# Performance work log

Hardware: AMD Instinct MI355X
Metric: run time of the kernel (lower is better)

## Reference

```python
import jax, jax.numpy as jnp
import numpy as np

N_NODES = 156
NFEAT = 256
NHID = 128
B = 16384
T = 24
HLSTM = 32
ALPHA = 0.2


def setup_inputs() -> dict:
    key = jax.random.key(0)
    ks = jax.random.split(key, 16)
    f32 = jnp.float32
    inp = {
        "embedding": jax.random.normal(ks[0], (N_NODES, NFEAT), f32),
        "x": jax.random.normal(ks[1], (B, T, N_NODES), f32),
        "adj": jax.random.randint(ks[2], (N_NODES, N_NODES), 0, 2, jnp.int32),
        # GAT params (xavier-ish scale)
        "W_recent": jax.random.normal(ks[3], (NFEAT, NHID), f32) * 0.08,
        "a_recent": jax.random.normal(ks[4], (2 * NHID, 1), f32) * 0.1,
        "W_period": jax.random.normal(ks[5], (NFEAT, NHID), f32) * 0.08,
        "a_period": jax.random.normal(ks[6], (2 * NHID, 1), f32) * 0.1,
        # LSTM params, torch layout: weight_ih [4H, D], weight_hh [4H, H]
        "Wih_r": jax.random.normal(ks[7], (4 * HLSTM, N_NODES), f32) * 0.08,
        "Whh_r": jax.random.normal(ks[8], (4 * HLSTM, HLSTM), f32) * 0.08,
        "bih_r": jnp.zeros((4 * HLSTM,), f32),
        "bhh_r": jnp.zeros((4 * HLSTM,), f32),
        "Wih_p": jax.random.normal(ks[9], (4 * HLSTM, N_NODES), f32) * 0.08,
        "Whh_p": jax.random.normal(ks[10], (4 * HLSTM, HLSTM), f32) * 0.08,
        "bih_p": jnp.zeros((4 * HLSTM,), f32),
        "bhh_p": jnp.zeros((4 * HLSTM,), f32),
        "fc_W": jax.random.normal(ks[11], (N_NODES, 2 * HLSTM), f32) * 0.1,
        "fc_b": jnp.zeros((N_NODES,), f32),
    }
    return inp


def _gat_attention(embedding, W, a, adj):
    # h = embedding @ W : [N, F]
    h = embedding @ W
    F = h.shape[1]
    # e[i,j] = leakyrelu(h_i . a[:F] + h_j . a[F:])  (same math as the
    # repeat/cat construction, without materializing [N*N, 2F])
    s1 = h @ a[:F, 0]   # [N]
    s2 = h @ a[F:, 0]   # [N]
    e = jax.nn.leaky_relu(s1[:, None] + s2[None, :], ALPHA)
    e = jnp.where(adj > 0, e, jnp.float32(-9e15))
    return jax.nn.softmax(e, axis=1)  # [N, N]


def _lstm_last(x_seq, Wih, Whh, bih, bhh):
    # x_seq: [B, T, D]; returns last hidden state [B, H]
    H = Whh.shape[1]
    Bn = x_seq.shape[0]
    h0 = jnp.zeros((Bn, H), x_seq.dtype)
    c0 = jnp.zeros((Bn, H), x_seq.dtype)
    bias = bih + bhh

    def step(carry, xt):
        h, c = carry
        g = xt @ Wih.T + h @ Whh.T + bias
        i, f, gg, o = jnp.split(g, 4, axis=-1)  # torch gate order i,f,g,o
        c = jax.nn.sigmoid(f) * c + jax.nn.sigmoid(i) * jnp.tanh(gg)
        h = jax.nn.sigmoid(o) * jnp.tanh(c)
        return (h, c), None

    (h, c), _ = jax.lax.scan(step, (h0, c0), jnp.swapaxes(x_seq, 0, 1))
    return h


def reference(embedding, x, adj, W_recent, a_recent, W_period, a_period,
              Wih_r, Whh_r, bih_r, bhh_r, Wih_p, Whh_p, bih_p, bhh_p,
              fc_W, fc_b):
    recent = x[:, :4, :]   # [B, 4, N]
    period = x[:, 4:, :]   # [B, T-4, N]

    # attention depends only on embedding/adj -> identical across timesteps
    attn_r = _gat_attention(embedding, W_recent, a_recent, adj)  # [N, N]
    attn_p = _gat_attention(embedding, W_period, a_period, adj)

    # out[b,t,i] = sum_j attn[i,j] * x[b,t,j]
    xr = jnp.einsum('ij,btj->bti', attn_r, recent)
    xp = jnp.einsum('ij,btj->bti', attn_p, period)

    hr = _lstm_last(xr, Wih_r, Whh_r, bih_r, bhh_r)  # [B, 32]
    hp = _lstm_last(xp, Wih_p, Whh_p, bih_p, bhh_p)  # [B, 32]

    h = jnp.concatenate([hr, hp], axis=1)            # [B, 64]
    return h @ fc_W.T + fc_b                         # [B, 156]
```

## Files before the change

### kernel.cpp

```cpp
#include <hip/hip_runtime.h>
#include <hip/hip_bf16.h>
#include <math.h>

#define N_NODES 156
#define NFEAT 256
#define NHID 128
#define BATCH 16384
#define TT 24
#define HLSTM 32
#define G4 128
#define ALPHA 0.2f
#define XSTRIDE (TT*N_NODES)
#define SLOTF 2496

typedef __attribute__((ext_vector_type(8))) short bf16x8;
typedef __attribute__((ext_vector_type(4))) float f32x4;

static __device__ __forceinline__ unsigned short f2bf(float f) {
    unsigned u = __float_as_uint(f);
    u += 0x7fffu + ((u >> 16) & 1u);
    return (unsigned short)(u >> 16);
}
static __device__ __forceinline__ bf16x8 cv8(float4 a, float4 b) {
    union { __hip_bfloat16 h[8]; bf16x8 v; } u;
    u.h[0] = __float2bfloat16(a.x); u.h[1] = __float2bfloat16(a.y);
    u.h[2] = __float2bfloat16(a.z); u.h[3] = __float2bfloat16(a.w);
    u.h[4] = __float2bfloat16(b.x); u.h[5] = __float2bfloat16(b.y);
    u.h[6] = __float2bfloat16(b.z); u.h[7] = __float2bfloat16(b.w);
    return u.v;
}
static __device__ __forceinline__ float sigm(float x) { return 1.f / (1.f + __expf(-x)); }
static __device__ __forceinline__ float tanh_(float x) { return 1.f - 2.f / (__expf(2.f * x) + 1.f); }

__global__ void k_gat_s(const float* __restrict__ emb,
                        const float* __restrict__ Wr, const float* __restrict__ ar,
                        const float* __restrict__ Wp, const float* __restrict__ ap,
                        float* __restrict__ s_buf ) {
    int i = blockIdx.x;
    int gat = blockIdx.y;
    const float* W = gat ? Wp : Wr;
    const float* a = gat ? ap : ar;
    int j = threadIdx.x;
    __shared__ float erow[NFEAT];
    __shared__ float red[128];
    for (int k = j; k < NFEAT; k += 128) erow[k] = emb[i*NFEAT + k];
    __syncthreads();
    float h = 0.f;
    for (int k = 0; k < NFEAT; ++k) h = fmaf(erow[k], W[k*NHID + j], h);
    float v1 = h * a[j];
    float v2 = h * a[NHID + j];
    red[j] = v1; __syncthreads();
    for (int s = 64; s > 0; s >>= 1) { if (j < s) red[j] += red[j+s]; __syncthreads(); }
    if (j == 0) s_buf[(gat*2+0)*N_NODES + i] = red[0];
    __syncthreads();
    red[j] = v2; __syncthreads();
    for (int s = 64; s > 0; s >>= 1) { if (j < s) red[j] += red[j+s]; __syncthreads(); }
    if (j == 0) s_buf[(gat*2+1)*N_NODES + i] = red[0];
}

__global__ void k_attn(const float* __restrict__ s_buf, const int* __restrict__ adj,
                       float* __restrict__ attn ) {
    int i = blockIdx.x, gat = blockIdx.y;
    int j = threadIdx.x;
    __shared__ float red[256];
    float s1 = s_buf[(gat*2+0)*N_NODES + i];
    bool act = (j < N_NODES);
    float e = -INFINITY;
    if (act) {
        float s2 = s_buf[(gat*2+1)*N_NODES + j];
        float z = s1 + s2;
        z = (z > 0.f) ? z : ALPHA * z;
        if (adj[i*N_NODES + j] <= 0) z = -9e15f;
        e = z;
    }
    red[j] = e; __syncthreads();
    for (int s = 128; s > 0; s >>= 1) { if (j < s) red[j] = fmaxf(red[j], red[j+s]); __syncthreads(); }
    float m = red[0]; __syncthreads();
    float val = act ? __expf(e - m) : 0.f;
    red[j] = val; __syncthreads();
    for (int s = 128; s > 0; s >>= 1) { if (j < s) red[j] += red[j+s]; __syncthreads(); }
    float inv = 1.f / red[0];
    if (act) attn[(gat*N_NODES + i)*N_NODES + j] = val * inv;
}

__global__ void k_prep(const float* __restrict__ attn,
                       const float* __restrict__ Wih_r, const float* __restrict__ Wih_p,
                       const float* __restrict__ Whh_r, const float* __restrict__ Whh_p,
                       const float* __restrict__ bih_r, const float* __restrict__ bhh_r,
                       const float* __restrict__ bih_p, const float* __restrict__ bhh_p,
                       unsigned short* __restrict__ Mbf ,
                       unsigned short* __restrict__ Whhbf ,
                       float* __restrict__ bias2 ) {
    int g = blockIdx.x, gat = blockIdx.y;
    const float* Wih = gat ? Wih_p : Wih_r;
    const float* A = attn + gat*N_NODES*N_NODES;
    int j = threadIdx.x;
    if (j < 160) {
        float acc = 0.f;
        if (j < N_NODES)
            for (int n = 0; n < N_NODES; ++n)
                acc = fmaf(Wih[g*N_NODES + n], A[n*N_NODES + j], acc);
        Mbf[(gat*G4 + g)*160 + j] = f2bf(acc);
    }
    if (j < HLSTM)
        Whhbf[(gat*G4 + g)*HLSTM + j] = f2bf((gat ? Whh_p : Whh_r)[g*HLSTM + j]);
    if (g == 0 && j < G4)
        bias2[gat*G4 + j] = gat ? (bih_p[j] + bhh_p[j]) : (bih_r[j] + bhh_r[j]);
}

__global__ void __launch_bounds__(128, 2)
k_fused(const float* __restrict__ x,
        const unsigned short* __restrict__ Mbf,
        const unsigned short* __restrict__ Whhbf,
        const float* __restrict__ bias2,
        const float* __restrict__ fcW,
        const float* __restrict__ fcb,
        float* __restrict__ out) {
    __shared__ __align__(16) float xsf[3][SLOTF];
    __shared__ __align__(16) unsigned short hfrag[512];
    __shared__ __align__(16) float P_ls[512];
    __shared__ __align__(16) unsigned short hcat[16*72];

    const int tid = threadIdx.x;
    const int w  = tid >> 6;
    const int l  = tid & 63;
    const int lm = l & 15;
    const int lg = l >> 4;
    const int b0 = blockIdx.x * 16;
    const float* xg = x + (size_t)b0 * XSTRIDE;

    unsigned goff[5];
    #pragma unroll
    for (int k = 0; k < 5; ++k) {
        int c = l + (w*5 + k)*64;
        if (c > 623) c = 623;
        int r = c / 39;
        goff[k] = (unsigned)(r*XSTRIDE + (c - r*39)*4);
    }

    bf16x8 bfr[4][5];
    bf16x8 wrec[4];
    float  bias_v[4];
    float  cst[8];
    unsigned short hrv[8], hpv[8];
    const int nbase = w ? 2 : 0;
    const float4 f4z = make_float4(0.f, 0.f, 0.f, 0.f);

#define LOAD_FRAGS(Mb, Wb, bs) do {                                          \
    _Pragma("unroll")                                                        \
    for (int nt = 0; nt < 4; ++nt) {                                         \
        int ntid = nbase + (nt & 1) + ((nt >> 1) << 2);                      \
        int n_ = ntid*16 + lm;                                               \
        _Pragma("unroll")                                                    \
        for (int kf = 0; kf < 5; ++kf)                                       \
            bfr[nt][kf] = *(const bf16x8*)((Mb) + n_*160 + kf*32 + lg*8);    \
        wrec[nt]   = *(const bf16x8*)((Wb) + n_*HLSTM + lg*8);               \
        bias_v[nt] = (bs)[n_];                                               \
    } } while (0)

#define DMA_STEP(S_, T_) do {                                                 \
    const float* gp_ = xg + (size_t)(T_)*N_NODES;                             \
    _Pragma("unroll")                                                         \
    for (int k_ = 0; k_ < 5; ++k_) {                                          \
        if (w*5 + k_ != 9 || l < 48)                                          \
            __builtin_amdgcn_global_load_lds(                                 \
                (const __attribute__((address_space(1))) void*)(gp_ + goff[k_]), \
                (__attribute__((address_space(3))) void*)(&xsf[S_][(w*5 + k_)*256]), \
                16, 0, 0);                                                    \
    } } while (0)

#define WAITVM(N_) asm volatile("s_waitcnt vmcnt(" #N_ ")" ::: "memory")
#define LGKM0()    asm volatile("s_waitcnt lgkmcnt(0)" ::: "memory")

    DMA_STEP(0, 0);
    LOAD_FRAGS(Mbf, Whhbf, bias2);
    DMA_STEP(1, 1);
    DMA_STEP(2, 2);

    if (w == 1) {
        #pragma unroll
        for (int ds = 0; ds < 2; ++ds)
            #pragma unroll
            for (int i = 0; i < 4; ++i) {
                hfrag[((lm>>3) + 2*ds)*128 + (lg*4 + i)*8 + (lm&7)] = 0;
                cst[ds*4 + i] = 0.f;
            }
    }

#define STEP(T_, S_, ISS_) do {                                               \
    LGKM0();                                                                  \
    __builtin_amdgcn_s_barrier();   \
    const float* xr_ = &xsf[S_][0] + lm*N_NODES + lg*8;                       \
    float4 q0_[5], q1_[5];                                                    \
    _Pragma("unroll")                                                         \
    for (int kf = 0; kf < 5; ++kf) {                                          \
        q0_[kf] = *(const float4*)(xr_ + kf*32);                              \
        q1_[kf] = *(const float4*)(xr_ + kf*32 + 4);                          \
    }                                                                         \
    bf16x8 hf_ = *(const bf16x8*)(hfrag + l*8);                               \
    if (lg == 3) q1_[4] = f4z;                       \
    bf16x8 af_[5];                                                            \
    _Pragma("unroll")                                                         \
    for (int kf = 0; kf < 5; ++kf) af_[kf] = cv8(q0_[kf], q1_[kf]);           \
    f32x4 acc[4];                                                             \
    _Pragma("unroll")                                                         \
    for (int nt = 0; nt < 4; ++nt)                                            \
        acc[nt] = (f32x4){bias_v[nt], bias_v[nt], bias_v[nt], bias_v[nt]};    \
    _Pragma("unroll")                                                         \
    for (int kf = 0; kf < 5; ++kf)                                            \
        _Pragma("unroll")                                                     \
        for (int nt = 0; nt < 4; ++nt)                                        \
            acc[nt] = __builtin_amdgcn_mfma_f32_16x16x32_bf16(af_[kf], bfr[nt][kf], acc[nt], 0, 0, 0); \
    _Pragma("unroll")                                                         \
    for (int nt = 0; nt < 4; ++nt)                                            \
        acc[nt] = __builtin_amdgcn_mfma_f32_16x16x32_bf16(hf_, wrec[nt], acc[nt], 0, 0, 0); \
    float sa_[8], sb_[8];                                                     \
    if (w == 0) {                                                             \
        _Pragma("unroll")                                                     \
        for (int ds = 0; ds < 2; ++ds)                                        \
            _Pragma("unroll")                                                 \
            for (int i = 0; i < 4; ++i) {                                     \
                float si = sigm(acc[ds][i]);                                  \
                float tg = tanh_(acc[2 + ds][i]);                             \
                P_ls[(ds*4 + i)*64 + l] = si * tg;                            \
            }                                                                 \
    } else {                                                                  \
        _Pragma("unroll")                                                     \
        for (int ds = 0; ds < 2; ++ds)                                        \
            _Pragma("unroll")                                                 \
            for (int i = 0; i < 4; ++i) {                                     \
                sa_[ds*4 + i] = sigm(acc[ds][i]);                     \
                sb_[ds*4 + i] = sigm(acc[2 + ds][i]);                 \
            }                                                                 \
    }                                                                         \
    LGKM0();                                                                  \
    __builtin_amdgcn_s_barrier();   \
    if (ISS_) DMA_STEP(S_, (T_) + 3);            \
    if (w == 1) {                                                             \
        _Pragma("unroll")                                                     \
        for (int ds = 0; ds < 2; ++ds)                                        \
            _Pragma("unroll")                                                 \
            for (int i = 0; i < 4; ++i) {                                     \
                int v = ds*4 + i;                                             \
                float c = sa_[v]*cst[v] + P_ls[v*64 + l];                     \
                float h = sb_[v]*tanh_(c);                                    \
                int cidx = ((lm>>3) + 2*ds)*128 + (lg*4 + i)*8 + (lm&7);      \
                if ((T_) == 3) {                \
                    hrv[v] = f2bf(h); hfrag[cidx] = 0; cst[v] = 0.f;          \
                } else if ((T_) == TT-1) {                                    \
                    hpv[v] = f2bf(h);                                         \
                } else {                                                      \
                    cst[v] = c; hfrag[cidx] = f2bf(h);                        \
                }                                                             \
            }                                                                 \
    }                                                                         \
    if ((T_) == 3) LOAD_FRAGS(Mbf + G4*160, Whhbf + G4*HLSTM, bias2 + G4);    \
    } while (0)

    for (int tb = 0; tb < 21; tb += 3) {
        WAITVM(10); STEP(tb + 0, 0, 1);
        WAITVM(10); STEP(tb + 1, 1, 1);
        WAITVM(10); STEP(tb + 2, 2, 1);
    }
    WAITVM(10); STEP(21, 0, 0);
    WAITVM(5);  STEP(22, 1, 0);
    WAITVM(0);  STEP(23, 2, 0);

    if (w == 1) {
        #pragma unroll
        for (int ds = 0; ds < 2; ++ds)
            #pragma unroll
            for (int i = 0; i < 4; ++i) {
                int r = lg*4 + i, d = lm + 16*ds, v = ds*4 + i;
                hcat[r*72 + d]      = hrv[v];
                hcat[r*72 + 32 + d] = hpv[v];
            }
    }
    LGKM0();
    __builtin_amdgcn_s_barrier();
    {
        bf16x8 ha0 = *(const bf16x8*)(hcat + lm*72 + lg*8);
        bf16x8 ha1 = *(const bf16x8*)(hcat + lm*72 + 32 + lg*8);
        #pragma unroll
        for (int nt5 = 0; nt5 < 5; ++nt5) {
            int nt = w*5 + nt5;
            int n  = nt*16 + lm;
            int nc = n < 155 ? n : 155;
            const float* wp0 = fcW + nc*64 + lg*8;
            const float* wp1 = fcW + nc*64 + 32 + lg*8;
            bf16x8 wf0 = cv8(*(const float4*)wp0, *(const float4*)(wp0 + 4));
            bf16x8 wf1 = cv8(*(const float4*)wp1, *(const float4*)(wp1 + 4));
            f32x4 fa = (f32x4){0.f, 0.f, 0.f, 0.f};
            fa = __builtin_amdgcn_mfma_f32_16x16x32_bf16(ha0, wf0, fa, 0, 0, 0);
            fa = __builtin_amdgcn_mfma_f32_16x16x32_bf16(ha1, wf1, fa, 0, 0, 0);
            if (n < N_NODES) {
                float bn = fcb[n];
                #pragma unroll
                for (int i = 0; i < 4; ++i)
                    out[(size_t)(b0 + lg*4 + i)*N_NODES + n] = fa[i] + bn;
            }
        }
    }
#undef STEP
#undef LGKM0
#undef WAITVM
#undef DMA_STEP
#undef LOAD_FRAGS
}

extern "C" void kernel_launch(void* const* d_in, const int* in_sizes, int n_in,
                              void* d_out, int out_size, void* d_ws, size_t ws_size,
                              hipStream_t stream) {
    (void)in_sizes; (void)n_in; (void)out_size; (void)ws_size;
    const float* emb   = (const float*)d_in[0];
    const float* x     = (const float*)d_in[1];
    const int*   adj   = (const int*)d_in[2];
    const float* Wr    = (const float*)d_in[3];
    const float* ar    = (const float*)d_in[4];
    const float* Wp    = (const float*)d_in[5];
    const float* ap    = (const float*)d_in[6];
    const float* Wih_r = (const float*)d_in[7];
    const float* Whh_r = (const float*)d_in[8];
    const float* bih_r = (const float*)d_in[9];
    const float* bhh_r = (const float*)d_in[10];
    const float* Wih_p = (const float*)d_in[11];
    const float* Whh_p = (const float*)d_in[12];
    const float* bih_p = (const float*)d_in[13];
    const float* bhh_p = (const float*)d_in[14];
    const float* fcW   = (const float*)d_in[15];
    const float* fcb   = (const float*)d_in[16];
    float* out = (float*)d_out;

    char* ws = (char*)d_ws;
    size_t off = 0;
    auto alloc = [&](size_t bytes) {
        char* p = ws + off;
        off += (bytes + 255) & ~(size_t)255;
        return p;
    };
    float*          attn  = (float*)alloc(2*156*156*sizeof(float));
    float*          sbuf  = (float*)alloc(4*156*sizeof(float));
    unsigned short* Mbf   = (unsigned short*)alloc(2*G4*160*sizeof(unsigned short));
    unsigned short* Whhbf = (unsigned short*)alloc(2*G4*HLSTM*sizeof(unsigned short));
    float*          bias2 = (float*)alloc(2*G4*sizeof(float));

    k_gat_s<<<dim3(156, 2), 128, 0, stream>>>(emb, Wr, ar, Wp, ap, sbuf);
    k_attn<<<dim3(156, 2), 256, 0, stream>>>(sbuf, adj, attn);
    k_prep<<<dim3(128, 2), 192, 0, stream>>>(attn, Wih_r, Wih_p, Whh_r, Whh_p,
                                             bih_r, bhh_r, bih_p, bhh_p,
                                             Mbf, Whhbf, bias2);
    k_fused<<<dim3(BATCH/16), 128, 0, stream>>>(x, Mbf, Whhbf, bias2, fcW, fcb, out);
}
```

Measured before the change: 102.6 us.

## Preload all timesteps as bf16 into LDS with 8 batch rows per block

Replaces the three-slot async global-to-LDS pipeline with an up-front load of the whole x slab for 8 batch rows, converted to bf16 and stored padded in LDS, followed by the 24 recurrent steps with no per-step DMA. The grid doubles to BATCH/8 blocks, each holding about 64KB of LDS, and launch bounds drop to one block per SIMD. Half of each 16-row MFMA tile is redundant, since rows are clamped to 8. This removes per-step vmcnt waits and fp32-to-bf16 conversion from the recurrent loop, at the cost of MFMA work per row, load/compute overlap within a block, and possibly occupancy.

```diff
diff --git a/kernel.cpp b/kernel.cpp
--- a/kernel.cpp
+++ b/kernel.cpp
@@ -10,8 +10,10 @@
 #define HLSTM 32
 #define G4 128
 #define ALPHA 0.2f
+#define ROWS 8
 #define XSTRIDE (TT*N_NODES)
-#define SLOTF 2496
+#define XROWPAD 168
+#define XT (ROWS*XROWPAD)
 
 typedef __attribute__((ext_vector_type(8))) short bf16x8;
 typedef __attribute__((ext_vector_type(4))) float f32x4;
@@ -108,7 +110,7 @@
         bias2[gat*G4 + j] = gat ? (bih_p[j] + bhh_p[j]) : (bih_r[j] + bhh_r[j]);
 }
 
-__global__ void __launch_bounds__(128, 2)
+__global__ void __launch_bounds__(128, 1)
 k_fused(const float* __restrict__ x,
         const unsigned short* __restrict__ Mbf,
         const unsigned short* __restrict__ Whhbf,
@@ -116,27 +118,17 @@
         const float* __restrict__ fcW,
         const float* __restrict__ fcb,
         float* __restrict__ out) {
-    __shared__ __align__(16) float xsf[3][SLOTF];
-    __shared__ __align__(16) unsigned short hfrag[512];
-    __shared__ __align__(16) float P_ls[512];
-    __shared__ __align__(16) unsigned short hcat[16*72];
+    __shared__ __align__(16) unsigned short xl[TT*XT];
+    __shared__ __align__(16) unsigned short hfr[ROWS*40];
+    __shared__ __align__(16) float P_ls[8*64];
 
     const int tid = threadIdx.x;
     const int w  = tid >> 6;
     const int l  = tid & 63;
     const int lm = l & 15;
     const int lg = l >> 4;
-    const int b0 = blockIdx.x * 16;
-    const float* xg = x + (size_t)b0 * XSTRIDE;
-
-    unsigned goff[5];
-    #pragma unroll
-    for (int k = 0; k < 5; ++k) {
-        int c = l + (w*5 + k)*64;
-        if (c > 623) c = 623;
-        int r = c / 39;
-        goff[k] = (unsigned)(r*XSTRIDE + (c - r*39)*4);
-    }
+    const int rl = (lm < ROWS) ? lm : (ROWS - 1);
+    const int b0 = blockIdx.x * ROWS;
 
     bf16x8 bfr[4][5];
     bf16x8 wrec[4];
@@ -144,7 +136,6 @@
     float  cst[8];
     unsigned short hrv[8], hpv[8];
     const int nbase = w ? 2 : 0;
-    const float4 f4z = make_float4(0.f, 0.f, 0.f, 0.f);
 
 #define LOAD_FRAGS(Mb, Wb, bs) do {                                          \
     _Pragma("unroll")                                                        \
@@ -158,50 +149,48 @@
         bias_v[nt] = (bs)[n_];                                               \
     } } while (0)
 
-#define DMA_STEP(S_, T_) do {                                                 \
-    const float* gp_ = xg + (size_t)(T_)*N_NODES;                             \
-    _Pragma("unroll")                                                         \
-    for (int k_ = 0; k_ < 5; ++k_) {                                          \
-        if (w*5 + k_ != 9 || l < 48)                                          \
-            __builtin_amdgcn_global_load_lds(                                 \
-                (const __attribute__((address_space(1))) void*)(gp_ + goff[k_]), \
-                (__attribute__((address_space(3))) void*)(&xsf[S_][(w*5 + k_)*256]), \
-                16, 0, 0);                                                    \
-    } } while (0)
-
-#define WAITVM(N_) asm volatile("s_waitcnt vmcnt(" #N_ ")" ::: "memory")
-#define LGKM0()    asm volatile("s_waitcnt lgkmcnt(0)" ::: "memory")
-
-    DMA_STEP(0, 0);
+#define LGKM0() asm volatile("s_waitcnt lgkmcnt(0)" ::: "memory")
+
     LOAD_FRAGS(Mbf, Whhbf, bias2);
-    DMA_STEP(1, 1);
-    DMA_STEP(2, 2);
-
-    if (w == 1) {
-        #pragma unroll
-        for (int ds = 0; ds < 2; ++ds)
-            #pragma unroll
-            for (int i = 0; i < 4; ++i) {
-                hfrag[((lm>>3) + 2*ds)*128 + (lg*4 + i)*8 + (lm&7)] = 0;
-                cst[ds*4 + i] = 0.f;
-            }
-    }
-
-#define STEP(T_, S_, ISS_) do {                                               \
+    #pragma unroll
+    for (int v = 0; v < 8; ++v) cst[v] = 0.f;
+
+    {
+        const float4* gsrc = (const float4*)(x + (size_t)b0 * XSTRIDE);
+#define STAGE1(FIDX) do {                                                     \
+        int f_ = (FIDX);                                                      \
+        float4 v_ = gsrc[f_];                                                 \
+        int row_ = f_ / 936;                                                  \
+        int rem_ = f_ - row_*936;                                             \
+        int t_   = rem_ / 39;                                                 \
+        int dq_  = rem_ - t_*39;                                              \
+        union { __hip_bfloat16 h[4]; uint2 u; } cv_;                          \
+        cv_.h[0] = __float2bfloat16(v_.x); cv_.h[1] = __float2bfloat16(v_.y); \
+        cv_.h[2] = __float2bfloat16(v_.z); cv_.h[3] = __float2bfloat16(v_.w); \
+        *(uint2*)(xl + t_*XT + row_*XROWPAD + dq_*4) = cv_.u;                 \
+    } while (0)
+        #pragma unroll 4
+        for (int j = 0; j < 58; ++j) STAGE1(j*128 + tid);
+        if (tid < 64) STAGE1(58*128 + tid);
+#undef STAGE1
+        uint2 z = make_uint2(0u, 0u);
+        if (tid < 192) { int t_ = tid >> 3, r_ = tid & 7;
+                         *(uint2*)(xl + t_*XT + r_*XROWPAD + 156) = z; }
+        { int i1 = tid + 128; if (i1 < 192) { int t_ = i1 >> 3, r_ = i1 & 7;
+                         *(uint2*)(xl + t_*XT + r_*XROWPAD + 156) = z; } }
+        if (tid < 80) *(uint2*)(hfr + tid*4) = z;
+    }
+    LGKM0();
+    __builtin_amdgcn_s_barrier();
+
+#define STEP(T_, STASH_, LAST_) do {                                          \
+    bf16x8 af_[5];                                                            \
+    { const unsigned short* xr_ = xl + (T_)*XT + rl*XROWPAD + lg*8;           \
+      _Pragma("unroll")                                                       \
+      for (int kf = 0; kf < 5; ++kf) af_[kf] = *(const bf16x8*)(xr_ + kf*32); } \
     LGKM0();                                                                  \
-    __builtin_amdgcn_s_barrier();   \
-    const float* xr_ = &xsf[S_][0] + lm*N_NODES + lg*8;                       \
-    float4 q0_[5], q1_[5];                                                    \
-    _Pragma("unroll")                                                         \
-    for (int kf = 0; kf < 5; ++kf) {                                          \
-        q0_[kf] = *(const float4*)(xr_ + kf*32);                              \
-        q1_[kf] = *(const float4*)(xr_ + kf*32 + 4);                          \
-    }                                                                         \
-    bf16x8 hf_ = *(const bf16x8*)(hfrag + l*8);                               \
-    if (lg == 3) q1_[4] = f4z;                       \
-    bf16x8 af_[5];                                                            \
-    _Pragma("unroll")                                                         \
-    for (int kf = 0; kf < 5; ++kf) af_[kf] = cv8(q0_[kf], q1_[kf]);           \
+    __builtin_amdgcn_s_barrier();                 \
+    bf16x8 hf_ = *(const bf16x8*)(hfr + rl*40 + lg*8);                        \
     f32x4 acc[4];                                                             \
     _Pragma("unroll")                                                         \
     for (int nt = 0; nt < 4; ++nt)                                            \
@@ -219,11 +208,8 @@
         _Pragma("unroll")                                                     \
         for (int ds = 0; ds < 2; ++ds)                                        \
             _Pragma("unroll")                                                 \
-            for (int i = 0; i < 4; ++i) {                                     \
-                float si = sigm(acc[ds][i]);                                  \
-                float tg = tanh_(acc[2 + ds][i]);                             \
-                P_ls[(ds*4 + i)*64 + l] = si * tg;                            \
-            }                                                                 \
+            for (int i = 0; i < 4; ++i)                                       \
+                P_ls[(ds*4 + i)*64 + l] = sigm(acc[ds][i]) * tanh_(acc[2 + ds][i]); \
     } else {                                                                  \
         _Pragma("unroll")                                                     \
         for (int ds = 0; ds < 2; ++ds)                                        \
@@ -234,9 +220,8 @@
             }                                                                 \
     }                                                                         \
     LGKM0();                                                                  \
-    __builtin_amdgcn_s_barrier();   \
-    if (ISS_) DMA_STEP(S_, (T_) + 3);            \
-    if (w == 1) {                                                             \
+    __builtin_amdgcn_s_barrier();                              \
+    if (w == 1 && lg < 2) {                                                   \
         _Pragma("unroll")                                                     \
         for (int ds = 0; ds < 2; ++ds)                                        \
             _Pragma("unroll")                                                 \
@@ -244,29 +229,26 @@
                 int v = ds*4 + i;                                             \
                 float c = sa_[v]*cst[v] + P_ls[v*64 + l];                     \
                 float h = sb_[v]*tanh_(c);                                    \
-                int cidx = ((lm>>3) + 2*ds)*128 + (lg*4 + i)*8 + (lm&7);      \
-                if ((T_) == 3) {                \
-                    hrv[v] = f2bf(h); hfrag[cidx] = 0; cst[v] = 0.f;          \
-                } else if ((T_) == TT-1) {                                    \
-                    hpv[v] = f2bf(h);                                         \
-                } else {                                                      \
-                    cst[v] = c; hfrag[cidx] = f2bf(h);                        \
-                }                                                             \
+                int r = lg*4 + i;                                             \
+                int d = lm + 16*ds;                                           \
+                if (STASH_) { hrv[v] = f2bf(h); hfr[r*40 + d] = 0; cst[v] = 0.f; } \
+                else if (LAST_) { hpv[v] = f2bf(h); }                         \
+                else { cst[v] = c; hfr[r*40 + d] = f2bf(h); }                 \
             }                                                                 \
     }                                                                         \
-    if ((T_) == 3) LOAD_FRAGS(Mbf + G4*160, Whhbf + G4*HLSTM, bias2 + G4);    \
     } while (0)
 
-    for (int tb = 0; tb < 21; tb += 3) {
-        WAITVM(10); STEP(tb + 0, 0, 1);
-        WAITVM(10); STEP(tb + 1, 1, 1);
-        WAITVM(10); STEP(tb + 2, 2, 1);
-    }
-    WAITVM(10); STEP(21, 0, 0);
-    WAITVM(5);  STEP(22, 1, 0);
-    WAITVM(0);  STEP(23, 2, 0);
-
-    if (w == 1) {
+    STEP(0, 0, 0);
+    STEP(1, 0, 0);
+    STEP(2, 0, 0);
+    STEP(3, 1, 0);
+    LOAD_FRAGS(Mbf + G4*160, Whhbf + G4*HLSTM, bias2 + G4);
+    #pragma unroll 1
+    for (int t = 4; t < TT-1; ++t) STEP(t, 0, 0);
+    STEP(TT-1, 0, 1);
+
+    unsigned short* hcat = (unsigned short*)P_ls;
+    if (w == 1 && lg < 2) {
         #pragma unroll
         for (int ds = 0; ds < 2; ++ds)
             #pragma unroll
@@ -279,8 +261,8 @@
     LGKM0();
     __builtin_amdgcn_s_barrier();
     {
-        bf16x8 ha0 = *(const bf16x8*)(hcat + lm*72 + lg*8);
-        bf16x8 ha1 = *(const bf16x8*)(hcat + lm*72 + 32 + lg*8);
+        bf16x8 ha0 = *(const bf16x8*)(hcat + rl*72 + lg*8);
+        bf16x8 ha1 = *(const bf16x8*)(hcat + rl*72 + 32 + lg*8);
         #pragma unroll
         for (int nt5 = 0; nt5 < 5; ++nt5) {
             int nt = w*5 + nt5;
@@ -293,7 +275,7 @@
             f32x4 fa = (f32x4){0.f, 0.f, 0.f, 0.f};
             fa = __builtin_amdgcn_mfma_f32_16x16x32_bf16(ha0, wf0, fa, 0, 0, 0);
             fa = __builtin_amdgcn_mfma_f32_16x16x32_bf16(ha1, wf1, fa, 0, 0, 0);
-            if (n < N_NODES) {
+            if (n < N_NODES && lg < 2) {
                 float bn = fcb[n];
                 #pragma unroll
                 for (int i = 0; i < 4; ++i)
@@ -303,8 +285,6 @@
     }
 #undef STEP
 #undef LGKM0
-#undef WAITVM
-#undef DMA_STEP
 #undef LOAD_FRAGS
 }
 
@@ -349,5 +329,5 @@
     k_prep<<<dim3(128, 2), 192, 0, stream>>>(attn, Wih_r, Wih_p, Whh_r, Whh_p,
                                              bih_r, bhh_r, bih_p, bhh_p,
                                              Mbf, Whhbf, bias2);
-    k_fused<<<dim3(BATCH/16), 128, 0, stream>>>(x, Mbf, Whhbf, bias2, fcW, fcb, out);
-}
+    k_fused<<<dim3(BATCH/ROWS), 128, 0, stream>>>(x, Mbf, Whhbf, bias2, fcW, fcb, out);
+}
```

Result: slower. 213.5 us (+108.1%).

## Stage x through registers as bf16 in padded LDS, double-buffered four-step groups

Applied to the files above, without the earlier changes.

Replaces the per-timestep async global-to-LDS DMA of fp32 x slices with register-staged loads that fetch four timesteps per row segment, convert to bf16 once, and write them into a padded, double-buffered bf16 LDS layout. The STEP macro then reads ready-made bf16 fragments instead of loading fp32 and converting per step. This is meant to shrink the LDS footprint, cut repeated conversion work and improve occupancy and coalescing. In exchange it uses many more registers for the staging buffers (va/vb) and depends on the compiler scheduling global loads across the barriers.

```diff
diff --git a/kernel.cpp b/kernel.cpp
--- a/kernel.cpp
+++ b/kernel.cpp
@@ -11,7 +11,8 @@
 #define G4 128
 #define ALPHA 0.2f
 #define XSTRIDE (TT*N_NODES)
-#define SLOTF 2496
+#define XROWPAD 168
+#define XT (16*XROWPAD)
 
 typedef __attribute__((ext_vector_type(8))) short bf16x8;
 typedef __attribute__((ext_vector_type(4))) float f32x4;
@@ -116,8 +117,8 @@
         const float* __restrict__ fcW,
         const float* __restrict__ fcb,
         float* __restrict__ out) {
-    __shared__ __align__(16) float xsf[3][SLOTF];
-    __shared__ __align__(16) unsigned short hfrag[512];
+    __shared__ __align__(16) unsigned short xb[2*4*XT];
+    __shared__ __align__(16) unsigned short hfr[512];
     __shared__ __align__(16) float P_ls[512];
     __shared__ __align__(16) unsigned short hcat[16*72];
 
@@ -127,16 +128,9 @@
     const int lm = l & 15;
     const int lg = l >> 4;
     const int b0 = blockIdx.x * 16;
-    const float* xg = x + (size_t)b0 * XSTRIDE;
-
-    unsigned goff[5];
-    #pragma unroll
-    for (int k = 0; k < 5; ++k) {
-        int c = l + (w*5 + k)*64;
-        if (c > 623) c = 623;
-        int r = c / 39;
-        goff[k] = (unsigned)(r*XSTRIDE + (c - r*39)*4);
-    }
+    const int srow = tid >> 3;
+    const int sseg = tid & 7;
+    const float* xrow = x + (size_t)(b0 + srow) * XSTRIDE;
 
     bf16x8 bfr[4][5];
     bf16x8 wrec[4];
@@ -144,7 +138,6 @@
     float  cst[8];
     unsigned short hrv[8], hpv[8];
     const int nbase = w ? 2 : 0;
-    const float4 f4z = make_float4(0.f, 0.f, 0.f, 0.f);
 
 #define LOAD_FRAGS(Mb, Wb, bs) do {                                          \
     _Pragma("unroll")                                                        \
@@ -158,50 +151,44 @@
         bias_v[nt] = (bs)[n_];                                               \
     } } while (0)
 
-#define DMA_STEP(S_, T_) do {                                                 \
-    const float* gp_ = xg + (size_t)(T_)*N_NODES;                             \
-    _Pragma("unroll")                                                         \
-    for (int k_ = 0; k_ < 5; ++k_) {                                          \
-        if (w*5 + k_ != 9 || l < 48)                                          \
-            __builtin_amdgcn_global_load_lds(                                 \
-                (const __attribute__((address_space(1))) void*)(gp_ + goff[k_]), \
-                (__attribute__((address_space(3))) void*)(&xsf[S_][(w*5 + k_)*256]), \
-                16, 0, 0);                                                    \
+#define LGKM0() asm volatile("s_waitcnt lgkmcnt(0)" ::: "memory")
+
+#define SLOAD(V_, G_, H_) do {                                                \
+    const float* rp_ = xrow + (size_t)(G_)*624;                               \
+    _Pragma("unroll")                                                         \
+    for (int k_ = 0; k_ < 10; ++k_) {                                         \
+        int kk_ = (H_)*10 + k_;                                               \
+        if (kk_ < 19)      V_[k_] = *(const float4*)(rp_ + (sseg + 8*kk_)*4); \
+        else if (sseg < 4) V_[k_] = *(const float4*)(rp_ + (sseg + 152)*4);   \
     } } while (0)
 
-#define WAITVM(N_) asm volatile("s_waitcnt vmcnt(" #N_ ")" ::: "memory")
-#define LGKM0()    asm volatile("s_waitcnt lgkmcnt(0)" ::: "memory")
-
-    DMA_STEP(0, 0);
-    LOAD_FRAGS(Mbf, Whhbf, bias2);
-    DMA_STEP(1, 1);
-    DMA_STEP(2, 2);
-
-    if (w == 1) {
-        #pragma unroll
-        for (int ds = 0; ds < 2; ++ds)
-            #pragma unroll
-            for (int i = 0; i < 4; ++i) {
-                hfrag[((lm>>3) + 2*ds)*128 + (lg*4 + i)*8 + (lm&7)] = 0;
-                cst[ds*4 + i] = 0.f;
-            }
-    }
-
-#define STEP(T_, S_, ISS_) do {                                               \
+#define SWRITE(V_, BUF_, H_) do {                                             \
+    _Pragma("unroll")                                                         \
+    for (int k_ = 0; k_ < 10; ++k_) {                                         \
+        int kk_ = (H_)*10 + k_;                                               \
+        if (kk_ < 19 || sseg < 4) {                                           \
+            int f4_ = (kk_ < 19) ? (sseg + 8*kk_) : (sseg + 152);             \
+            int col_ = 4*f4_;                                                 \
+            int ts_ = (col_ >= 468) ? 3 : (col_ >= 312) ? 2 :                 \
+                      (col_ >= 156) ? 1 : 0;                                  \
+            int dc_ = col_ - ts_*156;                                         \
+            union { __hip_bfloat16 h[4]; uint2 u; } cv_;                      \
+            cv_.h[0] = __float2bfloat16(V_[k_].x);                            \
+            cv_.h[1] = __float2bfloat16(V_[k_].y);                            \
+            cv_.h[2] = __float2bfloat16(V_[k_].z);                            \
+            cv_.h[3] = __float2bfloat16(V_[k_].w);                            \
+            *(uint2*)(xb + ((BUF_)*4 + ts_)*XT + srow*XROWPAD + dc_) = cv_.u; \
+        }                                                                     \
+    } } while (0)
+
+#define STEP(TS_, CUR_, STASH_, LAST_) do {                                   \
     LGKM0();                                                                  \
-    __builtin_amdgcn_s_barrier();   \
-    const float* xr_ = &xsf[S_][0] + lm*N_NODES + lg*8;                       \
-    float4 q0_[5], q1_[5];                                                    \
-    _Pragma("unroll")                                                         \
-    for (int kf = 0; kf < 5; ++kf) {                                          \
-        q0_[kf] = *(const float4*)(xr_ + kf*32);                              \
-        q1_[kf] = *(const float4*)(xr_ + kf*32 + 4);                          \
-    }                                                                         \
-    bf16x8 hf_ = *(const bf16x8*)(hfrag + l*8);                               \
-    if (lg == 3) q1_[4] = f4z;                       \
+    __builtin_amdgcn_s_barrier();               \
+    const unsigned short* xr_ = xb + ((CUR_)*4 + (TS_))*XT + lm*XROWPAD + lg*8; \
     bf16x8 af_[5];                                                            \
     _Pragma("unroll")                                                         \
-    for (int kf = 0; kf < 5; ++kf) af_[kf] = cv8(q0_[kf], q1_[kf]);           \
+    for (int kf = 0; kf < 5; ++kf) af_[kf] = *(const bf16x8*)(xr_ + kf*32);   \
+    bf16x8 hf_ = *(const bf16x8*)(hfr + l*8);                                 \
     f32x4 acc[4];                                                             \
     _Pragma("unroll")                                                         \
     for (int nt = 0; nt < 4; ++nt)                                            \
@@ -219,11 +206,8 @@
         _Pragma("unroll")                                                     \
         for (int ds = 0; ds < 2; ++ds)                                        \
             _Pragma("unroll")                                                 \
-            for (int i = 0; i < 4; ++i) {                                     \
-                float si = sigm(acc[ds][i]);                                  \
-                float tg = tanh_(acc[2 + ds][i]);                             \
-                P_ls[(ds*4 + i)*64 + l] = si * tg;                            \
-            }                                                                 \
+            for (int i = 0; i < 4; ++i)                                       \
+                P_ls[(ds*4 + i)*64 + l] = sigm(acc[ds][i]) * tanh_(acc[2 + ds][i]); \
     } else {                                                                  \
         _Pragma("unroll")                                                     \
         for (int ds = 0; ds < 2; ++ds)                                        \
@@ -234,8 +218,7 @@
             }                                                                 \
     }                                                                         \
     LGKM0();                                                                  \
-    __builtin_amdgcn_s_barrier();   \
-    if (ISS_) DMA_STEP(S_, (T_) + 3);            \
+    __builtin_amdgcn_s_barrier();       \
     if (w == 1) {                                                             \
         _Pragma("unroll")                                                     \
         for (int ds = 0; ds < 2; ++ds)                                        \
@@ -245,26 +228,53 @@
                 float c = sa_[v]*cst[v] + P_ls[v*64 + l];                     \
                 float h = sb_[v]*tanh_(c);                                    \
                 int cidx = ((lm>>3) + 2*ds)*128 + (lg*4 + i)*8 + (lm&7);      \
-                if ((T_) == 3) {                \
-                    hrv[v] = f2bf(h); hfrag[cidx] = 0; cst[v] = 0.f;          \
-                } else if ((T_) == TT-1) {                                    \
-                    hpv[v] = f2bf(h);                                         \
-                } else {                                                      \
-                    cst[v] = c; hfrag[cidx] = f2bf(h);                        \
-                }                                                             \
+                if (STASH_)      { hrv[v] = f2bf(h); hfr[cidx] = 0; cst[v] = 0.f; } \
+                else if (LAST_)  { hpv[v] = f2bf(h); }                        \
+                else             { cst[v] = c; hfr[cidx] = f2bf(h); }         \
             }                                                                 \
     }                                                                         \
-    if ((T_) == 3) LOAD_FRAGS(Mbf + G4*160, Whhbf + G4*HLSTM, bias2 + G4);    \
     } while (0)
 
-    for (int tb = 0; tb < 21; tb += 3) {
-        WAITVM(10); STEP(tb + 0, 0, 1);
-        WAITVM(10); STEP(tb + 1, 1, 1);
-        WAITVM(10); STEP(tb + 2, 2, 1);
-    }
-    WAITVM(10); STEP(21, 0, 0);
-    WAITVM(5);  STEP(22, 1, 0);
-    WAITVM(0);  STEP(23, 2, 0);
+    LOAD_FRAGS(Mbf, Whhbf, bias2);
+    #pragma unroll
+    for (int v = 0; v < 8; ++v) cst[v] = 0.f;
+    if (w == 1) {
+        #pragma unroll
+        for (int ds = 0; ds < 2; ++ds)
+            #pragma unroll
+            for (int i = 0; i < 4; ++i)
+                hfr[((lm>>3) + 2*ds)*128 + (lg*4 + i)*8 + (lm&7)] = 0;
+    }
+    *(uint2*)(xb + tid*XROWPAD + 156) = make_uint2(0u, 0u);
+
+    float4 va[10], vb[10];
+    SLOAD(va, 0, 0); SWRITE(va, 0, 0);
+    SLOAD(vb, 0, 1); SWRITE(vb, 0, 1);
+
+    SLOAD(va, 1, 0);
+    STEP(0, 0, 0, 0);
+    STEP(1, 0, 0, 0);
+    SWRITE(va, 1, 0); SLOAD(vb, 1, 1);
+    STEP(2, 0, 0, 0);
+    STEP(3, 0, 1, 0);
+    LOAD_FRAGS(Mbf + G4*160, Whhbf + G4*HLSTM, bias2 + G4);
+    SWRITE(vb, 1, 1);
+
+    for (int g = 1; g <= 4; ++g) {
+        int cur = g & 1, nxt = cur ^ 1;
+        SLOAD(va, g + 1, 0);
+        STEP(0, cur, 0, 0);
+        STEP(1, cur, 0, 0);
+        SWRITE(va, nxt, 0); SLOAD(vb, g + 1, 1);
+        STEP(2, cur, 0, 0);
+        STEP(3, cur, 0, 0);
+        SWRITE(vb, nxt, 1);
+    }
+
+    STEP(0, 1, 0, 0);
+    STEP(1, 1, 0, 0);
+    STEP(2, 1, 0, 0);
+    STEP(3, 1, 0, 1);
 
     if (w == 1) {
         #pragma unroll
@@ -302,9 +312,9 @@
         }
     }
 #undef STEP
+#undef SWRITE
+#undef SLOAD
 #undef LGKM0
-#undef WAITVM
-#undef DMA_STEP
 #undef LOAD_FRAGS
 }
 
```

New measurement: 155.0 us. 1.51x slower.
